# Performance work log

Hardware: AMD Instinct MI355X
Metric: run time of the kernel (lower is better)

Reference implementation:

```python
import jax, jax.numpy as jnp
import numpy as np

EPS = 1e-7  # K.epsilon()

def setup_inputs() -> dict:
    key = jax.random.key(0)
    k1, k2, k3 = jax.random.split(key, 3)
    B, T, D = 32, 2048, 512
    x = jax.random.normal(k1, (B, T, D), dtype=jnp.float32)
    W = jax.random.normal(k2, (D, D), dtype=jnp.float32) * (1.0 / np.sqrt(D))
    b = jnp.zeros((D,), dtype=jnp.float32)
    u = jax.random.normal(k3, (D,), dtype=jnp.float32) * (1.0 / np.sqrt(D))
    return {"x": x, "W": W, "b": b, "u": u}

def reference(x, W, b, u):
    # uit = tanh(x @ W + b)  -> [B, T, D]
    uit = jnp.tanh(jnp.einsum('btd,de->bte', x, W) + b)
    # scores: sum over feature dim of uit * u -> [B, T]
    ait = jnp.einsum('btd,d->bt', uit, u)
    # exp + normalize over T (no mask); matches original exp/sum form
    a = jnp.exp(ait)
    a = a / (jnp.sum(a, axis=1, keepdims=True) + EPS)
    # weighted sum pooling over T -> [B, D]
    return jnp.einsum('btd,bt->bd', x, a)
```

## Files before the change

### kernel.cpp

```cpp
#include <hip/hip_runtime.h>
#include <math.h>

#define D_DIM 512

typedef short short8v __attribute__((ext_vector_type(8)));
typedef unsigned short ushort8v __attribute__((ext_vector_type(8)));
typedef unsigned short ushort4v __attribute__((ext_vector_type(4)));
typedef float f32x16 __attribute__((ext_vector_type(16)));

__device__ inline unsigned short f2bf(float f) {
    union { float f; unsigned int u; } a; a.f = f;
    unsigned int u = a.u;
    unsigned int r = (u + 0x7fffu + ((u >> 16) & 1u)) >> 16;
    return (unsigned short)r;
}

__device__ inline float fast_tanh(float y) {
    float e2 = __expf(2.f * y);
    return 1.f - __fdividef(2.f, e2 + 1.f);
}

__device__ inline unsigned ldsaddr(const void* p) {
    return (unsigned)(size_t)(__attribute__((address_space(3))) const void*)p;
}

__global__ __launch_bounds__(1024) void wt_kernel(const float* __restrict__ W,
                                                  unsigned short* __restrict__ Wb2,
                                                  float* __restrict__ zero_base,
                                                  int zero_count) {
    __shared__ __align__(16) unsigned short lbuf[16384];
    const int s = blockIdx.x;
    const int tid = threadIdx.x;
    if (s == 0) {
        for (int i = tid; i < zero_count; i += 1024) zero_base[i] = 0.f;
    }
    #pragma unroll
    for (int i = 0; i < 4; ++i) {
        int flat = tid + i * 1024;
        int kr = flat >> 7;
        int e4 = (flat & 127) * 4;
        float4 v = *(const float4*)(W + (size_t)(s * 32 + kr) * D_DIM + e4);
        int ks = kr >> 4, half = (kr >> 3) & 1, j = kr & 7;
        float vv[4] = {v.x, v.y, v.z, v.w};
        #pragma unroll
        for (int q = 0; q < 4; ++q) {
            int e = e4 + q, g = e >> 5, nl = e & 31;
            lbuf[ks * 8192 + ((g * 2 + half) * 32 + nl) * 8 + j] = f2bf(vv[q]);
        }
    }
    __syncthreads();
    #pragma unroll
    for (int i = 0; i < 2; ++i) {
        int c = tid + i * 1024;
        *(ushort8v*)(Wb2 + (size_t)s * 16384 + c * 8) = *(const ushort8v*)&lbuf[c * 8];
    }
}

__device__ __forceinline__ void pack_store(unsigned short* xa, int row, int c4, float4 v) {
    int ks = c4 >> 4, hf = (c4 >> 3) & 1, j0 = c4 & 7;
    int mi = row >> 5, r5 = row & 31;
    ushort4v pk;
    pk[0] = f2bf(v.x); pk[1] = f2bf(v.y); pk[2] = f2bf(v.z); pk[3] = f2bf(v.w);
    *(ushort4v*)&xa[(((ks * 2 + mi) * 2 + hf) * 32 + r5) * 8 + j0] = pk;
}

__global__ __launch_bounds__(512, 2) void gemm_ait_fused(
    const float* __restrict__ x, const unsigned short* __restrict__ Wb2,
    const float* __restrict__ bias, const float* __restrict__ u,
    float* __restrict__ numer, float* __restrict__ denom, int T)
{
    __shared__ __align__(128) unsigned short xa[32768];
    __shared__ float rowpart[8][64];

    const int tid  = threadIdx.x;
    const int wave = tid >> 6;
    const int lane = tid & 63;
    const int half = lane >> 5;
    const int nl   = lane & 31;
    const int m0   = blockIdx.x * 64;

    f32x16 acc[2][2];
    #pragma unroll
    for (int mi = 0; mi < 2; ++mi)
        #pragma unroll
        for (int ni = 0; ni < 2; ++ni)
            #pragma unroll
            for (int r = 0; r < 16; ++r) acc[mi][ni][r] = 0.f;

    short8v a[2][2], b[3][2];

    const unsigned bvoff0 = (unsigned)(((wave * 4 + half) * 32 + nl) * 16);
    const unsigned abase = ldsaddr(&xa[0]) + (unsigned)(half * 512 + nl * 16);

    const float* x0 = x + (size_t)m0 * D_DIM;

    #pragma unroll
    for (int i = 0; i < 3; ++i) {
        unsigned vo = bvoff0 + (unsigned)(i * 16384);
        asm volatile("global_load_dwordx4 %0, %1, %2"
                     : "=v"(b[i][0]) : "v"(vo), "s"(Wb2) : "memory");
        asm volatile("global_load_dwordx4 %0, %1, %2 offset:1024"
                     : "=v"(b[i][1]) : "v"(vo), "s"(Wb2) : "memory");
    }

    #pragma unroll
    for (int i = 0; i < 16; ++i) {
        int chunk = tid + i * 512;
        int row = chunk >> 7;
        int c4  = (chunk & 127) * 4;
        float4 v = *(const float4*)(x0 + (size_t)row * D_DIM + c4);
        pack_store(xa, row, c4, v);
    }
    __syncthreads();

    asm volatile("ds_read_b128 %0, %1" : "=v"(a[0][0]) : "v"(abase) : "memory");
    asm volatile("ds_read_b128 %0, %1 offset:1024" : "=v"(a[0][1]) : "v"(abase) : "memory");

    #pragma unroll
    for (int s = 0; s < 32; ++s) {
        if (s < 30)      { asm volatile("s_waitcnt vmcnt(4)" ::: "memory"); }
        else if (s == 30){ asm volatile("s_waitcnt vmcnt(2)" ::: "memory"); }
        else             { asm volatile("s_waitcnt vmcnt(0)" ::: "memory"); }
        __builtin_amdgcn_sched_barrier(0);
        if (s + 1 < 32) {
            unsigned ao = abase + (unsigned)((s + 1) * 2048);
            asm volatile("ds_read_b128 %0, %1" : "=v"(a[(s + 1) & 1][0]) : "v"(ao) : "memory");
            asm volatile("ds_read_b128 %0, %1 offset:1024" : "=v"(a[(s + 1) & 1][1]) : "v"(ao) : "memory");
            asm volatile("s_waitcnt lgkmcnt(2)" ::: "memory");
        } else {
            asm volatile("s_waitcnt lgkmcnt(0)" ::: "memory");
        }
        __builtin_amdgcn_sched_barrier(0);
        __builtin_amdgcn_s_setprio(1);
        acc[0][0] = __builtin_amdgcn_mfma_f32_32x32x16_bf16(a[s & 1][0], b[s % 3][0], acc[0][0], 0, 0, 0);
        acc[0][1] = __builtin_amdgcn_mfma_f32_32x32x16_bf16(a[s & 1][0], b[s % 3][1], acc[0][1], 0, 0, 0);
        acc[1][0] = __builtin_amdgcn_mfma_f32_32x32x16_bf16(a[s & 1][1], b[s % 3][0], acc[1][0], 0, 0, 0);
        acc[1][1] = __builtin_amdgcn_mfma_f32_32x32x16_bf16(a[s & 1][1], b[s % 3][1], acc[1][1], 0, 0, 0);
        __builtin_amdgcn_s_setprio(0);
        if (s + 3 < 32) {
            unsigned vo = bvoff0 + (unsigned)((s + 3) * 16384);
            asm volatile("global_load_dwordx4 %0, %1, %2"
                         : "=v"(b[s % 3][0]) : "v"(vo), "s"(Wb2) : "memory");
            asm volatile("global_load_dwordx4 %0, %1, %2 offset:1024"
                         : "=v"(b[s % 3][1]) : "v"(vo), "s"(Wb2) : "memory");
        }
    }

    float rowsum[2][16];
    #pragma unroll
    for (int mi = 0; mi < 2; ++mi)
        #pragma unroll
        for (int r = 0; r < 16; ++r) rowsum[mi][r] = 0.f;

    #pragma unroll
    for (int mi = 0; mi < 2; ++mi) {
        #pragma unroll
        for (int ni = 0; ni < 2; ++ni) {
            int col = wave * 64 + ni * 32 + nl;
            float be = bias[col], ue = u[col];
            #pragma unroll
            for (int r = 0; r < 16; ++r)
                rowsum[mi][r] += fast_tanh(acc[mi][ni][r] + be) * ue;
        }
    }
    #pragma unroll
    for (int mi = 0; mi < 2; ++mi)
        #pragma unroll
        for (int r = 0; r < 16; ++r) {
            float v = rowsum[mi][r];
            v += __shfl_xor(v, 1, 64);
            v += __shfl_xor(v, 2, 64);
            v += __shfl_xor(v, 4, 64);
            v += __shfl_xor(v, 8, 64);
            v += __shfl_xor(v, 16, 64);
            rowsum[mi][r] = v;
        }
    if (nl == 0) {
        #pragma unroll
        for (int mi = 0; mi < 2; ++mi)
            #pragma unroll
            for (int r = 0; r < 16; ++r) {
                int row = mi * 32 + (r & 3) + 8 * (r >> 2) + 4 * half;
                rowpart[wave][row] = rowsum[mi][r];
            }
    }
    __syncthreads();

    const int bidx = m0 / T;
    float* evals = (float*)&xa[0];
    if (tid < 64) {
        float s = 0.f;
        #pragma unroll
        for (int w = 0; w < 8; ++w) s += rowpart[w][tid];
        float e = __expf(s);
        evals[tid] = e;
        float t = e;
        t += __shfl_xor(t, 1, 64);
        t += __shfl_xor(t, 2, 64);
        t += __shfl_xor(t, 4, 64);
        t += __shfl_xor(t, 8, 64);
        t += __shfl_xor(t, 16, 64);
        t += __shfl_xor(t, 32, 64);
        if (tid == 0) atomicAdd(denom + bidx, t);
    }
    __syncthreads();

    const int dg = tid >> 7;
    const int d4 = (tid & 127) << 2;
    const float* xp = x + (size_t)m0 * D_DIM + d4;
    float4 pacc = {0.f, 0.f, 0.f, 0.f};
    #pragma unroll 4
    for (int r = dg; r < 64; r += 4) {
        float e = evals[r];
        float4 xv = *(const float4*)(xp + (size_t)r * D_DIM);
        pacc.x += e * xv.x; pacc.y += e * xv.y;
        pacc.z += e * xv.z; pacc.w += e * xv.w;
    }
    float4* ptmp = (float4*)&xa[256];
    if (dg > 0) ptmp[(dg - 1) * 128 + (tid & 127)] = pacc;
    __syncthreads();
    if (dg == 0) {
        float4 o0 = ptmp[tid], o1 = ptmp[128 + tid], o2 = ptmp[256 + tid];
        float* np = numer + (size_t)bidx * D_DIM + d4;
        atomicAdd(np + 0, pacc.x + o0.x + o1.x + o2.x);
        atomicAdd(np + 1, pacc.y + o0.y + o1.y + o2.y);
        atomicAdd(np + 2, pacc.z + o0.z + o1.z + o2.z);
        atomicAdd(np + 3, pacc.w + o0.w + o1.w + o2.w);
    }
}

__global__ __launch_bounds__(128) void out_div_kernel(
    const float* __restrict__ numer, const float* __restrict__ denom,
    float* __restrict__ out)
{
    const int b = blockIdx.x;
    const int tid = threadIdx.x;
    float inv = 1.0f / (denom[b] + 1e-7f);
    float4 v = *(const float4*)(numer + (size_t)b * D_DIM + tid * 4);
    v.x *= inv; v.y *= inv; v.z *= inv; v.w *= inv;
    *(float4*)(out + (size_t)b * D_DIM + tid * 4) = v;
}

__global__ __launch_bounds__(256) void gemm_ait_f32(
    const float* __restrict__ x, const float* __restrict__ W,
    const float* __restrict__ bias, const float* __restrict__ u,
    float* __restrict__ ait)
{
    __shared__ float xsf[64][68];
    __shared__ float wshf[64][132];
    const int tid = threadIdx.x;
    const int tx = tid & 15, ty = tid >> 4;
    const int m0 = blockIdx.x * 64;
    float rowsum[4] = {0.f, 0.f, 0.f, 0.f};
    for (int e0 = 0; e0 < D_DIM; e0 += 128) {
        float acc[4][8];
        #pragma unroll
        for (int i = 0; i < 4; ++i)
            #pragma unroll
            for (int j = 0; j < 8; ++j) acc[i][j] = 0.f;
        for (int kc = 0; kc < D_DIM; kc += 64) {
            #pragma unroll
            for (int i = 0; i < 4; ++i) {
                int idx = tid + i * 256;
                int r = idx >> 4, c = (idx & 15) * 4;
                *(float4*)&xsf[r][c] = *(const float4*)(x + (size_t)(m0 + r) * D_DIM + kc + c);
            }
            #pragma unroll
            for (int i = 0; i < 8; ++i) {
                int idx = tid + i * 256;
                int r = idx >> 5, c = (idx & 31) * 4;
                *(float4*)&wshf[r][c] = *(const float4*)(W + (size_t)(kc + r) * D_DIM + e0 + c);
            }
            __syncthreads();
            #pragma unroll 4
            for (int k = 0; k < 64; ++k) {
                float xv[4];
                #pragma unroll
                for (int i = 0; i < 4; ++i) xv[i] = xsf[ty * 4 + i][k];
                float4 w0 = *(const float4*)&wshf[k][tx * 8];
                float4 w1 = *(const float4*)&wshf[k][tx * 8 + 4];
                #pragma unroll
                for (int i = 0; i < 4; ++i) {
                    acc[i][0] += xv[i] * w0.x; acc[i][1] += xv[i] * w0.y;
                    acc[i][2] += xv[i] * w0.z; acc[i][3] += xv[i] * w0.w;
                    acc[i][4] += xv[i] * w1.x; acc[i][5] += xv[i] * w1.y;
                    acc[i][6] += xv[i] * w1.z; acc[i][7] += xv[i] * w1.w;
                }
            }
            __syncthreads();
        }
        #pragma unroll
        for (int j = 0; j < 8; ++j) {
            int e = e0 + tx * 8 + j;
            float be = bias[e], ue = u[e];
            #pragma unroll
            for (int i = 0; i < 4; ++i) rowsum[i] += tanhf(acc[i][j] + be) * ue;
        }
    }
    float* red = &xsf[0][0];
    #pragma unroll
    for (int i = 0; i < 4; ++i) red[(ty * 4 + i) * 16 + tx] = rowsum[i];
    __syncthreads();
    if (tid < 64) {
        float s = 0.f;
        #pragma unroll
        for (int j = 0; j < 16; ++j) s += red[tid * 16 + j];
        ait[m0 + tid] = s;
    }
}

__global__ __launch_bounds__(256) void softmax_kernel(float* __restrict__ ait, int T)
{
    const int b = blockIdx.x;
    float* p = ait + (size_t)b * T;
    const int tid = threadIdx.x;
    float ev[8];
    float local = 0.f;
    #pragma unroll
    for (int i = 0; i < 8; ++i) {
        ev[i] = expf(p[tid + i * 256]);
        local += ev[i];
    }
    #pragma unroll
    for (int off = 32; off > 0; off >>= 1)
        local += __shfl_down(local, off, 64);
    __shared__ float wsum[4];
    const int wv = tid >> 6, lane = tid & 63;
    if (lane == 0) wsum[wv] = local;
    __syncthreads();
    float total = wsum[0] + wsum[1] + wsum[2] + wsum[3];
    float inv = 1.0f / (total + 1e-7f);
    #pragma unroll
    for (int i = 0; i < 8; ++i) p[tid + i * 256] = ev[i] * inv;
}

__global__ __launch_bounds__(256) void pool_atomic_kernel(
    const float* __restrict__ x, const float* __restrict__ a,
    float* __restrict__ out, int T)
{
    const int chunks = T >> 8;
    const int b = blockIdx.x / chunks;
    const int c = blockIdx.x % chunks;
    const int tid = threadIdx.x;
    const int th = tid >> 7;
    const int d = (tid & 127) * 4;
    const float* xp = x + ((size_t)b * T + c * 256) * D_DIM + d;
    const float* ap = a + (size_t)b * T + c * 256;
    float4 acc = {0.f, 0.f, 0.f, 0.f};
    #pragma unroll 8
    for (int t = th; t < 256; t += 2) {
        float s = ap[t];
        float4 xv = *(const float4*)(xp + (size_t)t * D_DIM);
        acc.x += xv.x * s; acc.y += xv.y * s;
        acc.z += xv.z * s; acc.w += xv.w * s;
    }
    __shared__ float4 tmp[128];
    if (th == 1) tmp[tid & 127] = acc;
    __syncthreads();
    if (th == 0) {
        float4 o = tmp[tid];
        float* op = out + (size_t)b * D_DIM + tid * 4;
        atomicAdd(op + 0, acc.x + o.x);
        atomicAdd(op + 1, acc.y + o.y);
        atomicAdd(op + 2, acc.z + o.z);
        atomicAdd(op + 3, acc.w + o.w);
    }
}

extern "C" void kernel_launch(void* const* d_in, const int* in_sizes, int n_in,
                              void* d_out, int out_size, void* d_ws, size_t ws_size,
                              hipStream_t stream)
{
    const float* x    = (const float*)d_in[0];
    const float* W    = (const float*)d_in[1];
    const float* bias = (const float*)d_in[2];
    const float* u    = (const float*)d_in[3];
    float* out = (float*)d_out;

    const int Dd = in_sizes[2];
    const int M  = in_sizes[0] / Dd;
    const int B  = out_size / Dd;
    const int T  = M / B;
    const int chunks = T >> 8;

    const size_t wb_bytes  = (size_t)Dd * Dd * sizeof(unsigned short);
    const size_t ait_bytes = (size_t)M * sizeof(float);

    if (ws_size >= wb_bytes + ait_bytes) {
        unsigned short* Wb2 = (unsigned short*)d_ws;
        float* numer = (float*)((char*)d_ws + wb_bytes);
        float* denom = numer + (size_t)B * Dd;
        const int zero_count = B * Dd + B;

        wt_kernel<<<dim3(16), dim3(1024), 0, stream>>>(W, Wb2, numer, zero_count);
        gemm_ait_fused<<<dim3(M / 64), dim3(512), 0, stream>>>(x, Wb2, bias, u,
                                                               numer, denom, T);
        out_div_kernel<<<dim3(B), dim3(128), 0, stream>>>(numer, denom, out);
    } else {
        float* ait = (float*)d_ws;
        gemm_ait_f32<<<dim3(M / 64), dim3(256), 0, stream>>>(x, W, bias, u, ait);
        softmax_kernel<<<dim3(B), dim3(256), 0, stream>>>(ait, T);
        hipMemsetAsync(d_out, 0, (size_t)out_size * sizeof(float), stream);
        pool_atomic_kernel<<<dim3(B * chunks), dim3(256), 0, stream>>>(x, ait, out, T);
    }
}
```

Before: 240.0 us.

## Pre-convert x to packed bf16 in a prep kernel and async-copy tiles into LDS

Adds a prep kernel that, alongside the W conversion, converts each 64-row x tile to bf16 in the MFMA-friendly packed layout and writes it to workspace. The GEMM kernel then loads its A tile straight into LDS with global_load_lds async copies, with no in-kernel conversion, and still re-reads fp32 x for the pooling step. This removes the conversion and packing work from the GEMM critical path. In exchange it adds an extra full pass over x, writing 64 MB of bf16 and reading it back, which may cost more than it saves on a memory-bound problem.

```diff
diff --git a/kernel.cpp b/kernel.cpp
--- a/kernel.cpp
+++ b/kernel.cpp
@@ -22,6 +22,44 @@
 
 __device__ inline unsigned ldsaddr(const void* p) {
     return (unsigned)(size_t)(__attribute__((address_space(3))) const void*)p;
+}
+
+#define ASYNC_CP16(gp, lp) \
+    __builtin_amdgcn_global_load_lds( \
+        (const __attribute__((address_space(1))) void*)(gp), \
+        (__attribute__((address_space(3))) void*)(lp), 16, 0, 0)
+
+__device__ __forceinline__ void pack_store(unsigned short* dst, int row, int c4, float4 v) {
+    int ks = c4 >> 4, hf = (c4 >> 3) & 1, j0 = c4 & 7;
+    int mi = row >> 5, r5 = row & 31;
+    ushort4v pk;
+    pk[0] = f2bf(v.x); pk[1] = f2bf(v.y); pk[2] = f2bf(v.z); pk[3] = f2bf(v.w);
+    *(ushort4v*)&dst[(((ks * 2 + mi) * 2 + hf) * 32 + r5) * 8 + j0] = pk;
+}
+
+__device__ __forceinline__ void wt_body(const float* __restrict__ W,
+                                        unsigned short* __restrict__ Wb2,
+                                        unsigned short* lbuf, int s, int tid) {
+    #pragma unroll
+    for (int i = 0; i < 4; ++i) {
+        int flat = tid + i * 1024;
+        int kr = flat >> 7;
+        int e4 = (flat & 127) * 4;
+        float4 v = *(const float4*)(W + (size_t)(s * 32 + kr) * D_DIM + e4);
+        int ks = kr >> 4, half = (kr >> 3) & 1, j = kr & 7;
+        float vv[4] = {v.x, v.y, v.z, v.w};
+        #pragma unroll
+        for (int q = 0; q < 4; ++q) {
+            int e = e4 + q, g = e >> 5, nl = e & 31;
+            lbuf[ks * 8192 + ((g * 2 + half) * 32 + nl) * 8 + j] = f2bf(vv[q]);
+        }
+    }
+    __syncthreads();
+    #pragma unroll
+    for (int i = 0; i < 2; ++i) {
+        int c = tid + i * 1024;
+        *(ushort8v*)(Wb2 + (size_t)s * 16384 + c * 8) = *(const ushort8v*)&lbuf[c * 8];
+    }
 }
 
 __global__ __launch_bounds__(1024) void wt_kernel(const float* __restrict__ W,
@@ -34,34 +72,203 @@
     if (s == 0) {
         for (int i = tid; i < zero_count; i += 1024) zero_base[i] = 0.f;
     }
+    wt_body(W, Wb2, lbuf, s, tid);
+}
+
+__global__ __launch_bounds__(1024) void prep_kernel(
+    const float* __restrict__ W, unsigned short* __restrict__ Wb2,
+    const float* __restrict__ x, unsigned short* __restrict__ Xb,
+    float* __restrict__ zero_base, int zero_count)
+{
+    __shared__ __align__(16) unsigned short lbuf[32768];
+    const int tid = threadIdx.x;
+    if (blockIdx.x < 16) {
+        const int s = blockIdx.x;
+        if (s == 0) {
+            for (int i = tid; i < zero_count; i += 1024) zero_base[i] = 0.f;
+        }
+        wt_body(W, Wb2, lbuf, s, tid);
+        return;
+    }
+    const int tile = blockIdx.x - 16;
+    const float* x0 = x + (size_t)tile * 64 * D_DIM;
+    unsigned short* xb0 = Xb + (size_t)tile * 32768;
+    #pragma unroll
+    for (int i = 0; i < 8; ++i) {
+        int chunk = tid + i * 1024;
+        int row = chunk >> 7;
+        int c4  = (chunk & 127) * 4;
+        float4 v = *(const float4*)(x0 + (size_t)row * D_DIM + c4);
+        pack_store(lbuf, row, c4, v);
+    }
+    __syncthreads();
     #pragma unroll
     for (int i = 0; i < 4; ++i) {
-        int flat = tid + i * 1024;
-        int kr = flat >> 7;
-        int e4 = (flat & 127) * 4;
-        float4 v = *(const float4*)(W + (size_t)(s * 32 + kr) * D_DIM + e4);
-        int ks = kr >> 4, half = (kr >> 3) & 1, j = kr & 7;
-        float vv[4] = {v.x, v.y, v.z, v.w};
-        #pragma unroll
-        for (int q = 0; q < 4; ++q) {
-            int e = e4 + q, g = e >> 5, nl = e & 31;
-            lbuf[ks * 8192 + ((g * 2 + half) * 32 + nl) * 8 + j] = f2bf(vv[q]);
-        }
-    }
-    __syncthreads();
+        int c = tid + i * 1024;
+        *(ushort8v*)(xb0 + c * 8) = *(const ushort8v*)&lbuf[c * 8];
+    }
+}
+
+__global__ __launch_bounds__(512, 2) void gemm_ait_xb(
+    const float* __restrict__ x, const unsigned short* __restrict__ Xb,
+    const unsigned short* __restrict__ Wb2,
+    const float* __restrict__ bias, const float* __restrict__ u,
+    float* __restrict__ numer, float* __restrict__ denom, int T)
+{
+    __shared__ __align__(128) unsigned short xa[32768];
+    __shared__ float rowpart[8][64];
+
+    const int tid  = threadIdx.x;
+    const int wave = tid >> 6;
+    const int lane = tid & 63;
+    const int half = lane >> 5;
+    const int nl   = lane & 31;
+    const int m0   = blockIdx.x * 64;
+
+    f32x16 acc[2][2];
+    #pragma unroll
+    for (int mi = 0; mi < 2; ++mi)
+        #pragma unroll
+        for (int ni = 0; ni < 2; ++ni)
+            #pragma unroll
+            for (int r = 0; r < 16; ++r) acc[mi][ni][r] = 0.f;
+
+    short8v a[2][2], b[2][2];
+
+    const unsigned bvoff0 = (unsigned)(((wave * 4 + half) * 32 + nl) * 16);
+    const unsigned abase = ldsaddr(&xa[0]) + (unsigned)(half * 512 + nl * 16);
+
+    const unsigned short* xb0 = Xb + (size_t)blockIdx.x * 32768;
+    #pragma unroll
+    for (int i = 0; i < 8; ++i)
+        ASYNC_CP16(xb0 + tid * 8 + i * 4096, &xa[tid * 8 + i * 4096]);
+
     #pragma unroll
     for (int i = 0; i < 2; ++i) {
-        int c = tid + i * 1024;
-        *(ushort8v*)(Wb2 + (size_t)s * 16384 + c * 8) = *(const ushort8v*)&lbuf[c * 8];
-    }
-}
-
-__device__ __forceinline__ void pack_store(unsigned short* xa, int row, int c4, float4 v) {
-    int ks = c4 >> 4, hf = (c4 >> 3) & 1, j0 = c4 & 7;
-    int mi = row >> 5, r5 = row & 31;
-    ushort4v pk;
-    pk[0] = f2bf(v.x); pk[1] = f2bf(v.y); pk[2] = f2bf(v.z); pk[3] = f2bf(v.w);
-    *(ushort4v*)&xa[(((ks * 2 + mi) * 2 + hf) * 32 + r5) * 8 + j0] = pk;
+        unsigned vo = bvoff0 + (unsigned)(i * 16384);
+        asm volatile("global_load_dwordx4 %0, %1, %2"
+                     : "=v"(b[i][0]) : "v"(vo), "s"(Wb2) : "memory");
+        asm volatile("global_load_dwordx4 %0, %1, %2 offset:1024"
+                     : "=v"(b[i][1]) : "v"(vo), "s"(Wb2) : "memory");
+    }
+
+    asm volatile("s_waitcnt vmcnt(4)" ::: "memory");
+    __builtin_amdgcn_sched_barrier(0);
+    __builtin_amdgcn_s_barrier();
+
+    asm volatile("ds_read_b128 %0, %1" : "=v"(a[0][0]) : "v"(abase) : "memory");
+    asm volatile("ds_read_b128 %0, %1 offset:1024" : "=v"(a[0][1]) : "v"(abase) : "memory");
+
+    #pragma unroll
+    for (int s = 0; s < 32; ++s) {
+        if (s < 31) { asm volatile("s_waitcnt vmcnt(2)" ::: "memory"); }
+        else        { asm volatile("s_waitcnt vmcnt(0)" ::: "memory"); }
+        __builtin_amdgcn_sched_barrier(0);
+        if (s + 1 < 32) {
+            unsigned ao = abase + (unsigned)((s + 1) * 2048);
+            asm volatile("ds_read_b128 %0, %1" : "=v"(a[(s + 1) & 1][0]) : "v"(ao) : "memory");
+            asm volatile("ds_read_b128 %0, %1 offset:1024" : "=v"(a[(s + 1) & 1][1]) : "v"(ao) : "memory");
+            asm volatile("s_waitcnt lgkmcnt(2)" ::: "memory");
+        } else {
+            asm volatile("s_waitcnt lgkmcnt(0)" ::: "memory");
+        }
+        __builtin_amdgcn_sched_barrier(0);
+        __builtin_amdgcn_s_setprio(1);
+        acc[0][0] = __builtin_amdgcn_mfma_f32_32x32x16_bf16(a[s & 1][0], b[s & 1][0], acc[0][0], 0, 0, 0);
+        acc[0][1] = __builtin_amdgcn_mfma_f32_32x32x16_bf16(a[s & 1][0], b[s & 1][1], acc[0][1], 0, 0, 0);
+        acc[1][0] = __builtin_amdgcn_mfma_f32_32x32x16_bf16(a[s & 1][1], b[s & 1][0], acc[1][0], 0, 0, 0);
+        acc[1][1] = __builtin_amdgcn_mfma_f32_32x32x16_bf16(a[s & 1][1], b[s & 1][1], acc[1][1], 0, 0, 0);
+        __builtin_amdgcn_s_setprio(0);
+        if (s + 2 < 32) {
+            unsigned vo = bvoff0 + (unsigned)((s + 2) * 16384);
+            asm volatile("global_load_dwordx4 %0, %1, %2"
+                         : "=v"(b[s & 1][0]) : "v"(vo), "s"(Wb2) : "memory");
+            asm volatile("global_load_dwordx4 %0, %1, %2 offset:1024"
+                         : "=v"(b[s & 1][1]) : "v"(vo), "s"(Wb2) : "memory");
+        }
+    }
+
+    float rowsum[2][16];
+    #pragma unroll
+    for (int mi = 0; mi < 2; ++mi)
+        #pragma unroll
+        for (int r = 0; r < 16; ++r) rowsum[mi][r] = 0.f;
+
+    #pragma unroll
+    for (int mi = 0; mi < 2; ++mi) {
+        #pragma unroll
+        for (int ni = 0; ni < 2; ++ni) {
+            int col = wave * 64 + ni * 32 + nl;
+            float be = bias[col], ue = u[col];
+            #pragma unroll
+            for (int r = 0; r < 16; ++r)
+                rowsum[mi][r] += fast_tanh(acc[mi][ni][r] + be) * ue;
+        }
+    }
+    #pragma unroll
+    for (int mi = 0; mi < 2; ++mi)
+        #pragma unroll
+        for (int r = 0; r < 16; ++r) {
+            float v = rowsum[mi][r];
+            v += __shfl_xor(v, 1, 64);
+            v += __shfl_xor(v, 2, 64);
+            v += __shfl_xor(v, 4, 64);
+            v += __shfl_xor(v, 8, 64);
+            v += __shfl_xor(v, 16, 64);
+            rowsum[mi][r] = v;
+        }
+    if (nl == 0) {
+        #pragma unroll
+        for (int mi = 0; mi < 2; ++mi)
+            #pragma unroll
+            for (int r = 0; r < 16; ++r) {
+                int row = mi * 32 + (r & 3) + 8 * (r >> 2) + 4 * half;
+                rowpart[wave][row] = rowsum[mi][r];
+            }
+    }
+    __syncthreads();
+
+    const int bidx = m0 / T;
+    float* evals = (float*)&xa[0];
+    if (tid < 64) {
+        float s = 0.f;
+        #pragma unroll
+        for (int w = 0; w < 8; ++w) s += rowpart[w][tid];
+        float e = __expf(s);
+        evals[tid] = e;
+        float t = e;
+        t += __shfl_xor(t, 1, 64);
+        t += __shfl_xor(t, 2, 64);
+        t += __shfl_xor(t, 4, 64);
+        t += __shfl_xor(t, 8, 64);
+        t += __shfl_xor(t, 16, 64);
+        t += __shfl_xor(t, 32, 64);
+        if (tid == 0) atomicAdd(denom + bidx, t);
+    }
+    __syncthreads();
+
+    const int dg = tid >> 7;
+    const int d4 = (tid & 127) << 2;
+    const float* xp = x + (size_t)m0 * D_DIM + d4;
+    float4 pacc = {0.f, 0.f, 0.f, 0.f};
+    #pragma unroll 4
+    for (int r = dg; r < 64; r += 4) {
+        float e = evals[r];
+        float4 xv = *(const float4*)(xp + (size_t)r * D_DIM);
+        pacc.x += e * xv.x; pacc.y += e * xv.y;
+        pacc.z += e * xv.z; pacc.w += e * xv.w;
+    }
+    float4* ptmp = (float4*)&xa[256];
+    if (dg > 0) ptmp[(dg - 1) * 128 + (tid & 127)] = pacc;
+    __syncthreads();
+    if (dg == 0) {
+        float4 o0 = ptmp[tid], o1 = ptmp[128 + tid], o2 = ptmp[256 + tid];
+        float* np = numer + (size_t)bidx * D_DIM + d4;
+        atomicAdd(np + 0, pacc.x + o0.x + o1.x + o2.x);
+        atomicAdd(np + 1, pacc.y + o0.y + o1.y + o2.y);
+        atomicAdd(np + 2, pacc.z + o0.z + o1.z + o2.z);
+        atomicAdd(np + 3, pacc.w + o0.w + o1.w + o2.w);
+    }
 }
 
 __global__ __launch_bounds__(512, 2) void gemm_ait_fused(
@@ -385,8 +592,22 @@
 
     const size_t wb_bytes  = (size_t)Dd * Dd * sizeof(unsigned short);
     const size_t ait_bytes = (size_t)M * sizeof(float);
-
-    if (ws_size >= wb_bytes + ait_bytes) {
+    const size_t xb_off    = 1u << 20;
+    const size_t xb_bytes  = (size_t)M * Dd * sizeof(unsigned short);
+
+    if (ws_size >= xb_off + xb_bytes) {
+        unsigned short* Wb2 = (unsigned short*)d_ws;
+        float* numer = (float*)((char*)d_ws + wb_bytes);
+        float* denom = numer + (size_t)B * Dd;
+        unsigned short* Xb = (unsigned short*)((char*)d_ws + xb_off);
+        const int zero_count = B * Dd + B;
+
+        prep_kernel<<<dim3(16 + M / 64), dim3(1024), 0, stream>>>(
+            W, Wb2, x, Xb, numer, zero_count);
+        gemm_ait_xb<<<dim3(M / 64), dim3(512), 0, stream>>>(
+            x, Xb, Wb2, bias, u, numer, denom, T);
+        out_div_kernel<<<dim3(B), dim3(128), 0, stream>>>(numer, denom, out);
+    } else if (ws_size >= wb_bytes + ait_bytes) {
         unsigned short* Wb2 = (unsigned short*)d_ws;
         float* numer = (float*)((char*)d_ws + wb_bytes);
         float* denom = numer + (size_t)B * Dd;
```

Result: slower. 272.7 us (+13.7%).
